# Kernel optimization log

Hardware: AMD Instinct MI355X
Metric: run time of the kernel (lower is better)

Reference implementation:

```python
import jax, jax.numpy as jnp
from jax import lax
import numpy as np

N = 227328   # B(32) * T(64) * 111 ROIs, block-diagonal collated graph
E = 1000000  # thresholded sparse edges
H = 128      # hidden_dim
NB = 111     # brain ROIs per graph (hardcoded in source)
P = 40       # |perm| (pooled node subset)
MAXLEN = 10  # max_path_length
NSTART = 5   # top-5 start nodes


def setup_inputs() -> dict:
    key = jax.random.key(0)
    ks = jax.random.split(key, 12)
    s = 1.0 / np.sqrt(H)
    return dict(
        v=jax.random.normal(ks[0], (N, H), jnp.float32),
        edge_row=jax.random.randint(ks[1], (E,), 0, N, jnp.int32),
        edge_col=jax.random.randint(ks[2], (E,), 0, N, jnp.int32),
        W1=jax.random.normal(ks[3], (H, H), jnp.float32) * s,
        b1=jnp.zeros((H,), jnp.float32),
        g1=jnp.ones((H,), jnp.float32),
        be1=jnp.zeros((H,), jnp.float32),
        W2=jax.random.normal(ks[4], (H, H), jnp.float32) * s,
        b2=jnp.zeros((H,), jnp.float32),
        g2=jnp.ones((H,), jnp.float32),
        be2=jnp.zeros((H,), jnp.float32),
        epsilon=jnp.zeros((1, 1), jnp.float32),
        adj111=jax.random.randint(ks[5], (NB, NB), 0, 2, jnp.int32),
        node_scores=jax.random.normal(ks[6], (NB,), jnp.float32),
        node_feats=jax.random.normal(ks[7], (NB, H), jnp.float32),
        perm=jnp.arange(P, dtype=jnp.int32),
        x_small=jax.random.normal(ks[8], (P, H), jnp.float32),
    )


def _batchnorm(x, g, b, eps=1e-5):
    # BatchNorm1d in training mode: biased batch statistics over node dim
    m = x.mean(0)
    var = x.var(0)
    return g * (x - m) * lax.rsqrt(var + eps) + b


def _gin(v, row, col, epsilon, W1, b1, g1, be1, W2, b2, g2, be2):
    # torch.sparse.mm(a, v): agg[i] = sum_{j: a[i,j]=1} v[j]
    agg = jax.ops.segment_sum(v[col], row, num_segments=v.shape[0])
    h = agg + epsilon[0, 0] * v
    h = jax.nn.relu(_batchnorm(h @ W1 + b1, g1, be1))
    h = jax.nn.relu(_batchnorm(h @ W2 + b2, g2, be2))
    return h


def _biased_random_walk(adj, scores, x, feats, perm):
    soft = jax.nn.softmax(scores)
    order = jnp.argsort(-scores)              # nodes by descending score
    in_perm = jnp.isin(order, perm)
    pos = jnp.where(in_perm, jnp.arange(NB), NB)
    starts = order[jnp.argsort(pos)[:NSTART]]  # first 5 sorted nodes in perm
    start_ok = jnp.arange(NSTART) < jnp.minimum(jnp.sum(in_perm), NSTART)

    def walk_one(carry, se):
        all_visited, xc = carry
        start, ok = se
        skip = jnp.logical_or(~ok, all_visited[start])
        visited0 = all_visited.at[start].set(True)

        def step(c, _):
            cur, visited, alive = c
            nbr = (adj[cur] > 0) & (~visited)
            has = jnp.any(nbr) & alive
            nxt = jnp.argmax(jnp.where(nbr, soft, -jnp.inf))  # greedy by softmax score
            cur2 = jnp.where(has, nxt, cur)
            visited2 = jnp.where(has, visited.at[nxt].set(True), visited)
            return (cur2, visited2, has), (cur2, has)

        (_, visited_f, _), (pn, pv) = lax.scan(
            step, (start, visited0, True), None, length=MAXLEN - 1)
        path = jnp.concatenate([start[None], pn])           # [MAXLEN]
        valid = jnp.concatenate([jnp.array([True]), pv])
        w = jax.nn.softmax(jnp.where(valid, scores[path], -jnp.inf))
        fused = jnp.sum(w[:, None] * feats[path], axis=0)   # [H]
        idx = jnp.argmax(perm == start)
        do = (~skip) & jnp.any(perm == start)
        x_new = jnp.where(do, xc.at[idx].add(fused), xc)
        av_new = jnp.where(skip, all_visited, visited_f)
        return (av_new, x_new), None

    (_, x_out), _ = lax.scan(
        walk_one, (jnp.zeros((NB,), bool), x), (starts, start_ok))
    return x_out


def reference(v, edge_row, edge_col, W1, b1, g1, be1, W2, b2, g2, be2,
              epsilon, adj111, node_scores, node_feats, perm, x_small):
    gin_out = _gin(v, edge_row, edge_col, epsilon,
                   W1, b1, g1, be1, W2, b2, g2, be2)
    x_fused = _biased_random_walk(adj111, node_scores, x_small,
                                  node_feats, perm)
    return gin_out, x_fused
```

## Files before the change

kernel.cpp:

```cpp
#include <hip/hip_runtime.h>
#include <hip/hip_bf16.h>
#include <math.h>

#define N_NODES 227328
#define H_DIM 128
#define NB_ 111
#define P_ 40
#define MAXLEN_ 10
#define NSTART_ 5
#define NH (N_NODES * H_DIM)
#define SCAN_BLK 1024

typedef __attribute__((ext_vector_type(8))) short short8;
typedef __attribute__((ext_vector_type(8))) unsigned short ushort8;
typedef __attribute__((ext_vector_type(4))) float f32x4;


__global__ __launch_bounds__(256) void k_zero(float* wsf, int* cnt, int n) {
    int gstride = gridDim.x * blockDim.x;
    for (int i = blockIdx.x * blockDim.x + threadIdx.x; i < n; i += gstride) cnt[i] = 0;
    if (blockIdx.x == 0)
        for (int i = threadIdx.x; i < 1280; i += 256) wsf[i] = 0.f;
}


__device__ inline unsigned short f2bf(float x) {
    unsigned u = __float_as_uint(x);
    return (unsigned short)((u + 0x7FFFu + ((u >> 16) & 1u)) >> 16);
}

__global__ __launch_bounds__(256) void k_conv(const float4* __restrict__ v4,
                                              ushort8* __restrict__ vb8, int n8) {
    int stride = gridDim.x * blockDim.x;
    for (int i = blockIdx.x * blockDim.x + threadIdx.x; i < n8; i += stride) {
        float4 a = v4[i * 2], b = v4[i * 2 + 1];
        ushort8 o;
        o[0] = f2bf(a.x); o[1] = f2bf(a.y); o[2] = f2bf(a.z); o[3] = f2bf(a.w);
        o[4] = f2bf(b.x); o[5] = f2bf(b.y); o[6] = f2bf(b.z); o[7] = f2bf(b.w);
        vb8[i] = o;
    }
}


__global__ __launch_bounds__(256) void k_hist(const int* __restrict__ erow, int* cnt, int E) {
    int stride = gridDim.x * blockDim.x;
    for (int e = blockIdx.x * blockDim.x + threadIdx.x; e < E; e += stride)
        atomicAdd(&cnt[erow[e]], 1);
}

__global__ __launch_bounds__(256) void k_scan1(const int* __restrict__ cnt, int* __restrict__ ptr,
                                               int* __restrict__ bsum, int n) {
    __shared__ int s_warp[4];
    int t = threadIdx.x;
    int base = blockIdx.x * SCAN_BLK + t * 4;
    int x0 = (base + 0 < n) ? cnt[base + 0] : 0;
    int x1 = (base + 1 < n) ? cnt[base + 1] : 0;
    int x2 = (base + 2 < n) ? cnt[base + 2] : 0;
    int x3 = (base + 3 < n) ? cnt[base + 3] : 0;
    int tsum = x0 + x1 + x2 + x3;
    int lane = t & 63, w = t >> 6;
    int v = tsum;
#pragma unroll
    for (int m = 1; m < 64; m <<= 1) {
        int o = __shfl_up(v, m, 64);
        if (lane >= m) v += o;
    }
    if (lane == 63) s_warp[w] = v;
    __syncthreads();
    int wadd = 0;
    for (int j = 0; j < w; j++) wadd += s_warp[j];
    int excl = v - tsum + wadd;
    if (base + 0 < n) ptr[base + 0] = excl;
    if (base + 1 < n) ptr[base + 1] = excl + x0;
    if (base + 2 < n) ptr[base + 2] = excl + x0 + x1;
    if (base + 3 < n) ptr[base + 3] = excl + x0 + x1 + x2;
    if (t == 0) bsum[blockIdx.x] = s_warp[0] + s_warp[1] + s_warp[2] + s_warp[3];
}

__global__ __launch_bounds__(256) void k_scan2(int* bsum, int nb) {
    __shared__ int s[256];
    int t = threadIdx.x;
    s[t] = (t < nb) ? bsum[t] : 0;
    __syncthreads();
    if (t == 0) {
        int acc = 0;
        for (int i = 0; i < nb; i++) { int x = s[i]; s[i] = acc; acc += x; }
    }
    __syncthreads();
    if (t < nb) bsum[t] = s[t];
}

__global__ __launch_bounds__(256) void k_scan3(int* __restrict__ ptr, const int* __restrict__ bsum,
                                               int* __restrict__ cur, int n, int E) {
    int stride = gridDim.x * blockDim.x;
    for (int i = blockIdx.x * blockDim.x + threadIdx.x; i < n; i += stride) {
        int p = ptr[i] + bsum[i / SCAN_BLK];
        ptr[i] = p;
        cur[i] = p;
    }
    if (blockIdx.x == 0 && threadIdx.x == 0) ptr[n] = E;
}

__global__ __launch_bounds__(256) void k_fill(const int* __restrict__ erow,
                                              const int* __restrict__ ecol,
                                              int* cur, int* __restrict__ col, int E) {
    int stride = gridDim.x * blockDim.x;
    for (int e = blockIdx.x * blockDim.x + threadIdx.x; e < E; e += stride) {
        int p = atomicAdd(&cur[erow[e]], 1);
        col[p] = ecol[e];
    }
}


__device__ inline float blo(unsigned u) { return __uint_as_float(u << 16); }
__device__ inline float bhi(unsigned u) { return __uint_as_float(u & 0xFFFF0000u); }

__global__ __launch_bounds__(256) void k_agg_bf16(const float* __restrict__ v,
                                                  const unsigned* __restrict__ vbu,
                                                  const int* __restrict__ ptr,
                                                  const int* __restrict__ col,
                                                  const float* __restrict__ epsp,
                                                  float* __restrict__ out, int n) {
    int r = (blockIdx.x * 256 + threadIdx.x) >> 6;
    int lane = threadIdx.x & 63;
    if (r >= n) return;
    float eps = epsp[0];
    float2 a = *((const float2*)(v + (size_t)r * H_DIM) + lane);
    float acx = eps * a.x, acy = eps * a.y;
    int s = ptr[r], e = ptr[r + 1];
    int i = s;
    for (; i + 8 <= e; i += 8) {
        unsigned u0 = vbu[(size_t)col[i + 0] * 64 + lane];
        unsigned u1 = vbu[(size_t)col[i + 1] * 64 + lane];
        unsigned u2 = vbu[(size_t)col[i + 2] * 64 + lane];
        unsigned u3 = vbu[(size_t)col[i + 3] * 64 + lane];
        unsigned u4 = vbu[(size_t)col[i + 4] * 64 + lane];
        unsigned u5 = vbu[(size_t)col[i + 5] * 64 + lane];
        unsigned u6 = vbu[(size_t)col[i + 6] * 64 + lane];
        unsigned u7 = vbu[(size_t)col[i + 7] * 64 + lane];
        acx += ((blo(u0) + blo(u1)) + (blo(u2) + blo(u3))) +
               ((blo(u4) + blo(u5)) + (blo(u6) + blo(u7)));
        acy += ((bhi(u0) + bhi(u1)) + (bhi(u2) + bhi(u3))) +
               ((bhi(u4) + bhi(u5)) + (bhi(u6) + bhi(u7)));
    }
    for (; i + 4 <= e; i += 4) {
        unsigned u0 = vbu[(size_t)col[i + 0] * 64 + lane];
        unsigned u1 = vbu[(size_t)col[i + 1] * 64 + lane];
        unsigned u2 = vbu[(size_t)col[i + 2] * 64 + lane];
        unsigned u3 = vbu[(size_t)col[i + 3] * 64 + lane];
        acx += (blo(u0) + blo(u1)) + (blo(u2) + blo(u3));
        acy += (bhi(u0) + bhi(u1)) + (bhi(u2) + bhi(u3));
    }
    for (; i < e; i++) {
        unsigned u = vbu[(size_t)col[i] * 64 + lane];
        acx += blo(u);
        acy += bhi(u);
    }
    *((float2*)(out + (size_t)r * H_DIM) + lane) = make_float2(acx, acy);
}

__global__ __launch_bounds__(256) void k_agg(const float* __restrict__ v,
                                             const int* __restrict__ ptr,
                                             const int* __restrict__ col,
                                             const float* __restrict__ epsp,
                                             float* __restrict__ out, int n) {
    int r = (blockIdx.x * 256 + threadIdx.x) >> 6;
    int lane = threadIdx.x & 63;
    if (r >= n) return;
    float eps = epsp[0];
    float2 a = *((const float2*)(v + (size_t)r * H_DIM) + lane);
    float acx = eps * a.x, acy = eps * a.y;
    int s = ptr[r], e = ptr[r + 1];
    int i = s;
    for (; i + 4 <= e; i += 4) {
        int c0 = col[i], c1 = col[i + 1], c2 = col[i + 2], c3 = col[i + 3];
        float2 b0 = *((const float2*)(v + (size_t)c0 * H_DIM) + lane);
        float2 b1 = *((const float2*)(v + (size_t)c1 * H_DIM) + lane);
        float2 b2 = *((const float2*)(v + (size_t)c2 * H_DIM) + lane);
        float2 b3 = *((const float2*)(v + (size_t)c3 * H_DIM) + lane);
        acx += (b0.x + b1.x) + (b2.x + b3.x);
        acy += (b0.y + b1.y) + (b2.y + b3.y);
    }
    for (; i < e; i++) {
        int c = col[i];
        float2 b = *((const float2*)(v + (size_t)c * H_DIM) + lane);
        acx += b.x;
        acy += b.y;
    }
    *((float2*)(out + (size_t)r * H_DIM) + lane) = make_float2(acx, acy);
}


__global__ __launch_bounds__(256) void k_init(const float4* __restrict__ v4,
                                              const float* __restrict__ epsp,
                                              float4* __restrict__ out4, int n4) {
    float eps = epsp[0];
    int stride = gridDim.x * blockDim.x;
    for (int i = blockIdx.x * blockDim.x + threadIdx.x; i < n4; i += stride) {
        float4 a = v4[i];
        out4[i] = make_float4(eps * a.x, eps * a.y, eps * a.z, eps * a.w);
    }
}

__global__ __launch_bounds__(256) void k_scatter(const float* __restrict__ v,
                                                 const int* __restrict__ erow,
                                                 const int* __restrict__ ecol,
                                                 float* agg, int E) {
    int tid = blockIdx.x * blockDim.x + threadIdx.x;
    int lane = tid & 63;
    int wave = tid >> 6;
    int nwaves = (gridDim.x * blockDim.x) >> 6;
    for (int e = wave; e < E; e += nwaves) {
        int r = erow[e], c = ecol[e];
        const float2 val = *((const float2*)(v + (size_t)c * H_DIM) + lane);
        float* dst = agg + (size_t)r * H_DIM + lane * 2;
        unsafeAtomicAdd(dst, val.x);
        unsafeAtomicAdd(dst + 1, val.y);
    }
}


template <int BN>
__global__ __launch_bounds__(256, 2) void k_gemm_mfma(
        const float* __restrict__ A, float* __restrict__ C,
        const float* __restrict__ W, const float* __restrict__ bias,
        const float* __restrict__ scl_in, const float* __restrict__ of_in,
        float* __restrict__ sums, float* __restrict__ sumsq) {
    __shared__ unsigned short Whi[128 * 136];
    __shared__ unsigned short Wlo[128 * 136];
    __shared__ float scof[256];
    __shared__ float stats[2][4][128];

    const int t = threadIdx.x;
    const int w = t >> 6;
    const int l = t & 63;
    const int n = l & 15;
    const int g = l >> 4;
    const size_t row0 = (size_t)blockIdx.x * 128 + w * 32;

    const float* Arow0 = A + (row0 + n) * H_DIM;
    const float* Arow1 = A + (row0 + 16 + n) * H_DIM;

    float4 x00 = *(const float4*)(Arow0 + g * 8);
    float4 x01 = *(const float4*)(Arow0 + g * 8 + 4);
    float4 x10 = *(const float4*)(Arow1 + g * 8);
    float4 x11 = *(const float4*)(Arow1 + g * 8 + 4);

#pragma unroll
    for (int it = 0; it < 8; ++it) {
        int p = it * 256 + t;
        int k = (p >> 5) * 2;
        int c = (p & 31) * 4;
        float4 wa = *(const float4*)(W + k * 128 + c);
        float4 wb = *(const float4*)(W + (k + 1) * 128 + c);
        float fa[4] = {wa.x, wa.y, wa.z, wa.w};
        float fb[4] = {wb.x, wb.y, wb.z, wb.w};
#pragma unroll
        for (int j = 0; j < 4; ++j) {
            unsigned ua = __float_as_uint(fa[j]);
            unsigned ub = __float_as_uint(fb[j]);
            unsigned ha = ua >> 16, hb = ub >> 16;
            float ra = fa[j] - __uint_as_float(ua & 0xFFFF0000u);
            float rb = fb[j] - __uint_as_float(ub & 0xFFFF0000u);
            unsigned la = __float_as_uint(ra) >> 16;
            unsigned lb = __float_as_uint(rb) >> 16;
            *(unsigned*)(&Whi[(c + j) * 136 + k]) = ha | (hb << 16);
            *(unsigned*)(&Wlo[(c + j) * 136 + k]) = la | (lb << 16);
        }
    }
    if (BN && t < 128) { scof[t] = scl_in[t]; scof[128 + t] = of_in[t]; }
    __syncthreads();

    float breg[8];
#pragma unroll
    for (int cb = 0; cb < 8; cb++) breg[cb] = bias[cb * 16 + n];

    f32x4 acc[2][8];
#pragma unroll
    for (int rf = 0; rf < 2; rf++)
#pragma unroll
        for (int cb = 0; cb < 8; cb++) acc[rf][cb] = (f32x4){0.f, 0.f, 0.f, 0.f};

#pragma unroll
    for (int kb = 0; kb < 4; kb++) {
        float4 y00, y01, y10, y11;
        if (kb < 3) {
            const int kn = (kb + 1) * 32 + g * 8;
            y00 = *(const float4*)(Arow0 + kn);
            y01 = *(const float4*)(Arow0 + kn + 4);
            y10 = *(const float4*)(Arow1 + kn);
            y11 = *(const float4*)(Arow1 + kn + 4);
        }
        const int k0 = kb * 32 + g * 8;
        float xs0[8] = {x00.x, x00.y, x00.z, x00.w, x01.x, x01.y, x01.z, x01.w};
        float xs1[8] = {x10.x, x10.y, x10.z, x10.w, x11.x, x11.y, x11.z, x11.w};
        if (BN) {
            float sc[8], of[8];
            float4 sa = *(const float4*)(scof + k0);
            float4 sb = *(const float4*)(scof + k0 + 4);
            float4 oa = *(const float4*)(scof + 128 + k0);
            float4 ob = *(const float4*)(scof + 128 + k0 + 4);
            sc[0] = sa.x; sc[1] = sa.y; sc[2] = sa.z; sc[3] = sa.w;
            sc[4] = sb.x; sc[5] = sb.y; sc[6] = sb.z; sc[7] = sb.w;
            of[0] = oa.x; of[1] = oa.y; of[2] = oa.z; of[3] = oa.w;
            of[4] = ob.x; of[5] = ob.y; of[6] = ob.z; of[7] = ob.w;
#pragma unroll
            for (int e = 0; e < 8; e++) {
                xs0[e] = fmaxf(fmaf(xs0[e], sc[e], of[e]), 0.f);
                xs1[e] = fmaxf(fmaf(xs1[e], sc[e], of[e]), 0.f);
            }
        }
        short8 ah0, al0, ah1, al1;
#pragma unroll
        for (int e = 0; e < 8; e++) {
            unsigned u0 = __float_as_uint(xs0[e]);
            ah0[e] = (short)(unsigned short)(u0 >> 16);
            al0[e] = (short)(unsigned short)(__float_as_uint(xs0[e] - __uint_as_float(u0 & 0xFFFF0000u)) >> 16);
            unsigned u1 = __float_as_uint(xs1[e]);
            ah1[e] = (short)(unsigned short)(u1 >> 16);
            al1[e] = (short)(unsigned short)(__float_as_uint(xs1[e] - __uint_as_float(u1 & 0xFFFF0000u)) >> 16);
        }

        short8 wh[8], wl[8];
        const int wb = n * 136 + kb * 32 + g * 8;
#pragma unroll
        for (int cb = 0; cb < 8; cb++) {
            wh[cb] = *(const short8*)(Whi + cb * 2176 + wb);
            wl[cb] = *(const short8*)(Wlo + cb * 2176 + wb);
        }
#pragma unroll
        for (int cb = 0; cb < 8; cb++) {
            acc[0][cb] = __builtin_amdgcn_mfma_f32_16x16x32_bf16(ah0, wh[cb], acc[0][cb], 0, 0, 0);
            acc[1][cb] = __builtin_amdgcn_mfma_f32_16x16x32_bf16(ah1, wh[cb], acc[1][cb], 0, 0, 0);
            acc[0][cb] = __builtin_amdgcn_mfma_f32_16x16x32_bf16(al0, wh[cb], acc[0][cb], 0, 0, 0);
            acc[1][cb] = __builtin_amdgcn_mfma_f32_16x16x32_bf16(al1, wh[cb], acc[1][cb], 0, 0, 0);
            acc[0][cb] = __builtin_amdgcn_mfma_f32_16x16x32_bf16(ah0, wl[cb], acc[0][cb], 0, 0, 0);
            acc[1][cb] = __builtin_amdgcn_mfma_f32_16x16x32_bf16(ah1, wl[cb], acc[1][cb], 0, 0, 0);
        }
        x00 = y00; x01 = y01; x10 = y10; x11 = y11;
    }

    float s[8], s2[8];
#pragma unroll
    for (int cb = 0; cb < 8; cb++) { s[cb] = 0.f; s2[cb] = 0.f; }
#pragma unroll
    for (int cb = 0; cb < 8; cb++) {
        const int c = cb * 16 + n;
#pragma unroll
        for (int rf = 0; rf < 2; rf++) {
            f32x4 o = acc[rf][cb];
            const size_t rbase = (row0 + rf * 16 + g * 4) * H_DIM + c;
#pragma unroll
            for (int r = 0; r < 4; r++) {
                float val = o[r] + breg[cb];
                C[rbase + (size_t)r * H_DIM] = val;
                s[cb] += val;
                s2[cb] += val * val;
            }
        }
    }
#pragma unroll
    for (int cb = 0; cb < 8; cb++) {
        s[cb] += __shfl_xor(s[cb], 16, 64);
        s[cb] += __shfl_xor(s[cb], 32, 64);
        s2[cb] += __shfl_xor(s2[cb], 16, 64);
        s2[cb] += __shfl_xor(s2[cb], 32, 64);
    }
    if (g == 0) {
#pragma unroll
        for (int cb = 0; cb < 8; cb++) {
            stats[0][w][cb * 16 + n] = s[cb];
            stats[1][w][cb * 16 + n] = s2[cb];
        }
    }
    __syncthreads();
    if (t < 128) {
        float S  = stats[0][0][t] + stats[0][1][t] + stats[0][2][t] + stats[0][3][t];
        float S2 = stats[1][0][t] + stats[1][1][t] + stats[1][2][t] + stats[1][3][t];
        unsafeAtomicAdd(sums + t, S);
        unsafeAtomicAdd(sumsq + t, S2);
    }
}

__global__ void k_finalize(const float* __restrict__ sums, const float* __restrict__ sumsq,
                           float* __restrict__ mean, float* __restrict__ scl,
                           float* __restrict__ of,
                           const float* __restrict__ g, const float* __restrict__ beta,
                           float invN) {
    int t = threadIdx.x;
    if (t < H_DIM) {
        float m = sums[t] * invN;
        float var = sumsq[t] * invN - m * m;
        float sc = g[t] * rsqrtf(var + 1e-5f);
        mean[t] = m;
        scl[t] = sc;
        of[t] = beta[t] - m * sc;
    }
}


__device__ inline float block_max4(float v, int t, float* s_r) {
#pragma unroll
    for (int m = 1; m < 64; m <<= 1) v = fmaxf(v, __shfl_xor(v, m, 64));
    if ((t & 63) == 0) s_r[t >> 6] = v;
    __syncthreads();
    float r = fmaxf(fmaxf(s_r[0], s_r[1]), fmaxf(s_r[2], s_r[3]));
    __syncthreads();
    return r;
}

__device__ inline float block_sum4(float v, int t, float* s_r) {
#pragma unroll
    for (int m = 1; m < 64; m <<= 1) v += __shfl_xor(v, m, 64);
    if ((t & 63) == 0) s_r[t >> 6] = v;
    __syncthreads();
    float r = (s_r[0] + s_r[1]) + (s_r[2] + s_r[3]);
    __syncthreads();
    return r;
}

__device__ inline void block_argmax4(float v, int idx, int t, float* s_rv, int* s_ri,
                                     float* outv, int* outi) {
#pragma unroll
    for (int m = 1; m < 64; m <<= 1) {
        float ov = __shfl_xor(v, m, 64);
        int oi = __shfl_xor(idx, m, 64);
        if (ov > v || (ov == v && oi < idx)) { v = ov; idx = oi; }
    }
    if ((t & 63) == 0) { s_rv[t >> 6] = v; s_ri[t >> 6] = idx; }
    __syncthreads();
    float bv = s_rv[0];
    int bi = s_ri[0];
#pragma unroll
    for (int j = 1; j < 4; j++) {
        float ov = s_rv[j];
        int oi = s_ri[j];
        if (ov > bv || (ov == bv && oi < bi)) { bv = ov; bi = oi; }
    }
    *outv = bv;
    *outi = bi;
    __syncthreads();
}

__global__ __launch_bounds__(256) void k_bnwalk(
        float4* y4, const float* __restrict__ scl, const float* __restrict__ of, int n4,
        const int* __restrict__ adj, const float* __restrict__ scores,
        const float* __restrict__ feats, const int* __restrict__ perm,
        const float* __restrict__ xs, float* __restrict__ outw) {
    __shared__ int s_adj[NB_ * NB_];
    __shared__ float s_scores[NB_], s_soft[NB_];
    __shared__ int s_perm[P_];
    __shared__ unsigned char s_inperm[NB_], s_sel[NB_], s_allvis[NB_], s_vis[NB_];
    __shared__ int s_starts[NSTART_];
    __shared__ int s_path[MAXLEN_];
    __shared__ unsigned char s_valid[MAXLEN_];
    __shared__ float s_w[MAXLEN_];
    __shared__ int s_cur, s_alive, s_do, s_idx, s_skip;
    __shared__ float s_rv[4];
    __shared__ int s_ri[4];

    const int t = threadIdx.x;

    if (blockIdx.x != 0) {
        int stride = (gridDim.x - 1) * 256;
        for (int i = (blockIdx.x - 1) * 256 + t; i < n4; i += stride) {
            int c = (i & 31) * 4;
            float4 a = y4[i];
            a.x = fmaxf(fmaf(a.x, scl[c + 0], of[c + 0]), 0.f);
            a.y = fmaxf(fmaf(a.y, scl[c + 1], of[c + 1]), 0.f);
            a.z = fmaxf(fmaf(a.z, scl[c + 2], of[c + 2]), 0.f);
            a.w = fmaxf(fmaf(a.w, scl[c + 3], of[c + 3]), 0.f);
            y4[i] = a;
        }
        return;
    }

    for (int i = t; i < P_ * H_DIM; i += 256) outw[i] = xs[i];
    for (int i = t; i < NB_ * NB_; i += 256) s_adj[i] = adj[i];
    if (t < P_) s_perm[t] = perm[t];
    if (t < NB_) { s_scores[t] = scores[t]; s_allvis[t] = 0; s_sel[t] = 0; }
    __syncthreads();
    if (t < NB_) {
        unsigned char inp = 0;
        for (int j = 0; j < P_; j++) inp |= (s_perm[j] == t) ? 1 : 0;
        s_inperm[t] = inp;
    }
    __syncthreads();

    float myv = (t < NB_) ? s_scores[t] : -INFINITY;
    float mx = block_max4(myv, t, s_rv);
    float e = (t < NB_) ? expf(s_scores[t] - mx) : 0.f;
    float ssum = block_sum4(e, t, s_rv);
    if (t < NB_) s_soft[t] = e / ssum;

    float ninf = block_sum4((t < NB_ && s_inperm[t]) ? 1.f : 0.f, t, s_rv);
    int nin = (int)(ninf + 0.5f);
    int nok = nin < NSTART_ ? nin : NSTART_;
    __syncthreads();

    for (int r = 0; r < NSTART_; r++) {
        bool useIn = (r < nin);
        bool elig = (t < NB_) && !s_sel[t] && (((s_inperm[t] != 0)) == useIn);
        float v = elig ? s_scores[t] : -INFINITY;
        float mv; int mi;
        block_argmax4(v, elig ? t : 0x7fffffff, t, s_rv, s_ri, &mv, &mi);
        if (t == 0) s_starts[r] = mi;
        if (t == mi && t < NB_) s_sel[t] = 1;
        __syncthreads();
    }

    for (int s = 0; s < NSTART_; s++) {
        if (t == 0) {
            int start = s_starts[s];
            int ok = (s < nok) ? 1 : 0;
            int skip = (!ok) || s_allvis[start];
            s_skip = skip;
            s_cur = start;
            s_alive = 1;
            s_path[0] = start;
            s_valid[0] = 1;
            int idx = 0, found = 0;
            for (int j = 0; j < P_; j++)
                if (!found && s_perm[j] == start) { idx = j; found = 1; }
            s_idx = idx;
            s_do = (!skip) && found;
        }
        __syncthreads();
        if (t < NB_) s_vis[t] = s_allvis[t];
        __syncthreads();
        if (t == 0) s_vis[s_cur] = 1;
        __syncthreads();

        for (int st = 1; st < MAXLEN_; st++) {
            int cur = s_cur;
            int alive = s_alive;
            bool elig = (t < NB_) && alive && (s_adj[cur * NB_ + t] > 0) && (!s_vis[t]);
            float v = elig ? s_soft[t] : -INFINITY;
            float mv; int mi;
            block_argmax4(v, elig ? t : 0x7fffffff, t, s_rv, s_ri, &mv, &mi);
            if (t == 0) {
                int has = (mv > -INFINITY) ? 1 : 0;
                if (has) { s_cur = mi; s_vis[mi] = 1; }
                s_path[st] = has ? mi : cur;
                s_valid[st] = (unsigned char)has;
                s_alive = has;
            }
            __syncthreads();
        }

        if (t == 0) {
            float mxw = -INFINITY;
            for (int st = 0; st < MAXLEN_; st++)
                if (s_valid[st]) mxw = fmaxf(mxw, s_scores[s_path[st]]);
            float sw = 0.f;
            for (int st = 0; st < MAXLEN_; st++) {
                float ev = s_valid[st] ? expf(s_scores[s_path[st]] - mxw) : 0.f;
                s_w[st] = ev; sw += ev;
            }
            float inv = 1.f / sw;
            for (int st = 0; st < MAXLEN_; st++) s_w[st] *= inv;
        }
        __syncthreads();
        if (s_do && t < H_DIM) {
            float acc = 0.f;
            for (int st = 0; st < MAXLEN_; st++)
                acc += s_w[st] * feats[s_path[st] * H_DIM + t];
            outw[s_idx * H_DIM + t] += acc;
        }
        __syncthreads();
        if (!s_skip && t < NB_) s_allvis[t] = s_vis[t];
        __syncthreads();
    }
}


extern "C" void kernel_launch(void* const* d_in, const int* in_sizes, int n_in,
                              void* d_out, int out_size, void* d_ws, size_t ws_size,
                              hipStream_t stream) {
    const float* v    = (const float*)d_in[0];
    const int*   erow = (const int*)d_in[1];
    const int*   ecol = (const int*)d_in[2];
    const float* W1   = (const float*)d_in[3];
    const float* b1   = (const float*)d_in[4];
    const float* g1   = (const float*)d_in[5];
    const float* be1  = (const float*)d_in[6];
    const float* W2   = (const float*)d_in[7];
    const float* b2   = (const float*)d_in[8];
    const float* g2   = (const float*)d_in[9];
    const float* be2  = (const float*)d_in[10];
    const float* epsp = (const float*)d_in[11];
    const int*   adj  = (const int*)d_in[12];
    const float* scr  = (const float*)d_in[13];
    const float* fts  = (const float*)d_in[14];
    const int*   perm = (const int*)d_in[15];
    const float* xs   = (const float*)d_in[16];

    float* out = (float*)d_out;
    float* wsf = (float*)d_ws;
    float* sums1 = wsf,        *sumsq1 = wsf + 128,  *mean1 = wsf + 256,  *scl1 = wsf + 384,  *of1 = wsf + 512;
    float* sums2 = wsf + 640,  *sumsq2 = wsf + 768,  *mean2 = wsf + 896,  *scl2 = wsf + 1024, *of2 = wsf + 1152;

    const int E  = in_sizes[1];
    const int N  = N_NODES;
    const int n4 = NH / 4;

    int* ws_i = (int*)(wsf + 1280);
    int* cnt  = ws_i;
    int* ptr  = ws_i + (N + 1);
    int* cur  = ws_i + 2 * (N + 1);
    int* col  = ws_i + 3 * (N + 1);
    size_t need_csr = 1280 * 4 + (size_t)(3 * (N + 1) + E) * 4;
    size_t off_vb   = (need_csr + 15) & ~(size_t)15;
    size_t need_vb  = off_vb + (size_t)NH * 2;
    unsigned* vbu = (unsigned*)((char*)d_ws + off_vb);

    if (ws_size >= need_csr) {
        const int nb = (N + SCAN_BLK - 1) / SCAN_BLK;
        k_zero<<<512, 256, 0, stream>>>(wsf, cnt, N + 1);
        bool useBf = (ws_size >= need_vb);
        if (useBf)
            k_conv<<<2048, 256, 0, stream>>>((const float4*)v, (ushort8*)vbu, NH / 8);
        k_hist<<<1024, 256, 0, stream>>>(erow, cnt, E);
        k_scan1<<<nb, 256, 0, stream>>>(cnt, ptr, cur , N);
        k_scan2<<<1, 256, 0, stream>>>(cur, nb);
        k_scan3<<<512, 256, 0, stream>>>(ptr, cur, cnt , N, E);
        k_fill<<<1024, 256, 0, stream>>>(erow, ecol, cnt, col, E);
        if (useBf)
            k_agg_bf16<<<N / 4, 256, 0, stream>>>(v, vbu, ptr, col, epsp, out, N);
        else
            k_agg<<<N / 4, 256, 0, stream>>>(v, ptr, col, epsp, out, N);
    } else {
        k_zero<<<512, 256, 0, stream>>>(wsf, cnt, 0);
        k_init<<<2048, 256, 0, stream>>>((const float4*)v, epsp, (float4*)out, n4);
        k_scatter<<<4096, 256, 0, stream>>>(v, erow, ecol, out, E);
    }

    k_gemm_mfma<0><<<N / 128, 256, 0, stream>>>(out, out, W1, b1, nullptr, nullptr,
                                                sums1, sumsq1);
    k_finalize<<<1, 128, 0, stream>>>(sums1, sumsq1, mean1, scl1, of1, g1, be1, 1.f / N);
    k_gemm_mfma<1><<<N / 128, 256, 0, stream>>>(out, out, W2, b2, scl1, of1,
                                                sums2, sumsq2);
    k_finalize<<<1, 128, 0, stream>>>(sums2, sumsq2, mean2, scl2, of2, g2, be2, 1.f / N);
    k_bnwalk<<<2049, 256, 0, stream>>>((float4*)out, scl2, of2, n4,
                                       adj, scr, fts, perm, xs, out + NH);
}
```

Before: 712.9 us.

## Fuse histogram into bf16 conversion, simplify GEMM loads, bitmask adjacency in walk

Merges the edge-count histogram into the bf16 conversion kernel, removing one launch. The GEMM now stages W with scalar per-element loads instead of vectorized float4 loads, and reads A inside the k-loop instead of prefetching the next slice. The random walk packs the 111x111 adjacency into per-row 64-bit bitmasks, shrinking shared memory. The GEMM changes may lose load latency hiding and load efficiency, while the fusion and bitmask changes trim launch overhead and shared-memory use.

Measured after the change: 675.0 us. 5.3% less time.

```diff
diff --git a/kernel.cpp b/kernel.cpp
--- a/kernel.cpp
+++ b/kernel.cpp
@@ -29,24 +29,22 @@
     return (unsigned short)((u + 0x7FFFu + ((u >> 16) & 1u)) >> 16);
 }
 
-__global__ __launch_bounds__(256) void k_conv(const float4* __restrict__ v4,
-                                              ushort8* __restrict__ vb8, int n8) {
+__global__ __launch_bounds__(256) void k_hist_conv(const int* __restrict__ erow, int* cnt, int E,
+                                                   const float4* __restrict__ v4,
+                                                   ushort8* __restrict__ vb8, int n8) {
     int stride = gridDim.x * blockDim.x;
-    for (int i = blockIdx.x * blockDim.x + threadIdx.x; i < n8; i += stride) {
+    int tid = blockIdx.x * blockDim.x + threadIdx.x;
+    for (int i = tid; i < n8; i += stride) {
         float4 a = v4[i * 2], b = v4[i * 2 + 1];
         ushort8 o;
         o[0] = f2bf(a.x); o[1] = f2bf(a.y); o[2] = f2bf(a.z); o[3] = f2bf(a.w);
         o[4] = f2bf(b.x); o[5] = f2bf(b.y); o[6] = f2bf(b.z); o[7] = f2bf(b.w);
         vb8[i] = o;
     }
-}
-
-
-__global__ __launch_bounds__(256) void k_hist(const int* __restrict__ erow, int* cnt, int E) {
-    int stride = gridDim.x * blockDim.x;
-    for (int e = blockIdx.x * blockDim.x + threadIdx.x; e < E; e += stride)
+    for (int e = tid; e < E; e += stride)
         atomicAdd(&cnt[erow[e]], 1);
 }
+
 
 __global__ __launch_bounds__(256) void k_scan1(const int* __restrict__ cnt, int* __restrict__ ptr,
                                                int* __restrict__ bsum, int n) {
@@ -220,6 +218,16 @@
 }
 
 
+__device__ inline void split8(const float* xs, short8& hi, short8& lo) {
+#pragma unroll
+    for (int e = 0; e < 8; e++) {
+        unsigned u = __float_as_uint(xs[e]);
+        hi[e] = (short)(unsigned short)(u >> 16);
+        float hf = __uint_as_float(u & 0xFFFF0000u);
+        lo[e] = (short)(unsigned short)(__float_as_uint(xs[e] - hf) >> 16);
+    }
+}
+
 template <int BN>
 __global__ __launch_bounds__(256, 2) void k_gemm_mfma(
         const float* __restrict__ A, float* __restrict__ C,
@@ -238,60 +246,39 @@
     const int g = l >> 4;
     const size_t row0 = (size_t)blockIdx.x * 128 + w * 32;
 
+#pragma unroll 8
+    for (int it = 0; it < 64; ++it) {
+        int k = it * 2 + (t >> 7);
+        int nn = t & 127;
+        float wv = W[k * 128 + nn];
+        unsigned u = __float_as_uint(wv);
+        Whi[nn * 136 + k] = (unsigned short)(u >> 16);
+        float hf = __uint_as_float(u & 0xFFFF0000u);
+        Wlo[nn * 136 + k] = (unsigned short)(__float_as_uint(wv - hf) >> 16);
+    }
+    if (BN && t < 128) { scof[t] = scl_in[t]; scof[128 + t] = of_in[t]; }
+    __syncthreads();
+
+    float breg[8];
+#pragma unroll
+    for (int cb = 0; cb < 8; cb++) breg[cb] = bias[cb * 16 + n];
+
+    f32x4 acc[2][8];
+#pragma unroll
+    for (int rf = 0; rf < 2; rf++)
+#pragma unroll
+        for (int cb = 0; cb < 8; cb++) acc[rf][cb] = (f32x4){0.f, 0.f, 0.f, 0.f};
+
     const float* Arow0 = A + (row0 + n) * H_DIM;
     const float* Arow1 = A + (row0 + 16 + n) * H_DIM;
 
-    float4 x00 = *(const float4*)(Arow0 + g * 8);
-    float4 x01 = *(const float4*)(Arow0 + g * 8 + 4);
-    float4 x10 = *(const float4*)(Arow1 + g * 8);
-    float4 x11 = *(const float4*)(Arow1 + g * 8 + 4);
-
-#pragma unroll
-    for (int it = 0; it < 8; ++it) {
-        int p = it * 256 + t;
-        int k = (p >> 5) * 2;
-        int c = (p & 31) * 4;
-        float4 wa = *(const float4*)(W + k * 128 + c);
-        float4 wb = *(const float4*)(W + (k + 1) * 128 + c);
-        float fa[4] = {wa.x, wa.y, wa.z, wa.w};
-        float fb[4] = {wb.x, wb.y, wb.z, wb.w};
-#pragma unroll
-        for (int j = 0; j < 4; ++j) {
-            unsigned ua = __float_as_uint(fa[j]);
-            unsigned ub = __float_as_uint(fb[j]);
-            unsigned ha = ua >> 16, hb = ub >> 16;
-            float ra = fa[j] - __uint_as_float(ua & 0xFFFF0000u);
-            float rb = fb[j] - __uint_as_float(ub & 0xFFFF0000u);
-            unsigned la = __float_as_uint(ra) >> 16;
-            unsigned lb = __float_as_uint(rb) >> 16;
-            *(unsigned*)(&Whi[(c + j) * 136 + k]) = ha | (hb << 16);
-            *(unsigned*)(&Wlo[(c + j) * 136 + k]) = la | (lb << 16);
-        }
-    }
-    if (BN && t < 128) { scof[t] = scl_in[t]; scof[128 + t] = of_in[t]; }
-    __syncthreads();
-
-    float breg[8];
-#pragma unroll
-    for (int cb = 0; cb < 8; cb++) breg[cb] = bias[cb * 16 + n];
-
-    f32x4 acc[2][8];
-#pragma unroll
-    for (int rf = 0; rf < 2; rf++)
-#pragma unroll
-        for (int cb = 0; cb < 8; cb++) acc[rf][cb] = (f32x4){0.f, 0.f, 0.f, 0.f};
-
 #pragma unroll
     for (int kb = 0; kb < 4; kb++) {
-        float4 y00, y01, y10, y11;
-        if (kb < 3) {
-            const int kn = (kb + 1) * 32 + g * 8;
-            y00 = *(const float4*)(Arow0 + kn);
-            y01 = *(const float4*)(Arow0 + kn + 4);
-            y10 = *(const float4*)(Arow1 + kn);
-            y11 = *(const float4*)(Arow1 + kn + 4);
-        }
         const int k0 = kb * 32 + g * 8;
+        float4 x00 = *(const float4*)(Arow0 + k0);
+        float4 x01 = *(const float4*)(Arow0 + k0 + 4);
+        float4 x10 = *(const float4*)(Arow1 + k0);
+        float4 x11 = *(const float4*)(Arow1 + k0 + 4);
         float xs0[8] = {x00.x, x00.y, x00.z, x00.w, x01.x, x01.y, x01.z, x01.w};
         float xs1[8] = {x10.x, x10.y, x10.z, x10.w, x11.x, x11.y, x11.z, x11.w};
         if (BN) {
@@ -311,15 +298,8 @@
             }
         }
         short8 ah0, al0, ah1, al1;
-#pragma unroll
-        for (int e = 0; e < 8; e++) {
-            unsigned u0 = __float_as_uint(xs0[e]);
-            ah0[e] = (short)(unsigned short)(u0 >> 16);
-            al0[e] = (short)(unsigned short)(__float_as_uint(xs0[e] - __uint_as_float(u0 & 0xFFFF0000u)) >> 16);
-            unsigned u1 = __float_as_uint(xs1[e]);
-            ah1[e] = (short)(unsigned short)(u1 >> 16);
-            al1[e] = (short)(unsigned short)(__float_as_uint(xs1[e] - __uint_as_float(u1 & 0xFFFF0000u)) >> 16);
-        }
+        split8(xs0, ah0, al0);
+        split8(xs1, ah1, al1);
 
         short8 wh[8], wl[8];
         const int wb = n * 136 + kb * 32 + g * 8;
@@ -337,7 +317,6 @@
             acc[0][cb] = __builtin_amdgcn_mfma_f32_16x16x32_bf16(ah0, wl[cb], acc[0][cb], 0, 0, 0);
             acc[1][cb] = __builtin_amdgcn_mfma_f32_16x16x32_bf16(ah1, wl[cb], acc[1][cb], 0, 0, 0);
         }
-        x00 = y00; x01 = y01; x10 = y10; x11 = y11;
     }
 
     float s[8], s2[8];
@@ -447,7 +426,7 @@
         const int* __restrict__ adj, const float* __restrict__ scores,
         const float* __restrict__ feats, const int* __restrict__ perm,
         const float* __restrict__ xs, float* __restrict__ outw) {
-    __shared__ int s_adj[NB_ * NB_];
+    __shared__ unsigned long long s_am0[NB_], s_am1[NB_];
     __shared__ float s_scores[NB_], s_soft[NB_];
     __shared__ int s_perm[P_];
     __shared__ unsigned char s_inperm[NB_], s_sel[NB_], s_allvis[NB_], s_vis[NB_];
@@ -476,9 +455,17 @@
     }
 
     for (int i = t; i < P_ * H_DIM; i += 256) outw[i] = xs[i];
-    for (int i = t; i < NB_ * NB_; i += 256) s_adj[i] = adj[i];
     if (t < P_) s_perm[t] = perm[t];
     if (t < NB_) { s_scores[t] = scores[t]; s_allvis[t] = 0; s_sel[t] = 0; }
+    if (t < NB_) {
+        const int* row = adj + t * NB_;
+        unsigned long long m0 = 0ull, m1 = 0ull;
+#pragma unroll
+        for (int j = 0; j < 64; j++) m0 |= (unsigned long long)(row[j] > 0 ? 1u : 0u) << j;
+        for (int j = 64; j < NB_; j++) m1 |= (unsigned long long)(row[j] > 0 ? 1u : 0u) << (j - 64);
+        s_am0[t] = m0;
+        s_am1[t] = m1;
+    }
     __syncthreads();
     if (t < NB_) {
         unsigned char inp = 0;
@@ -534,7 +521,9 @@
         for (int st = 1; st < MAXLEN_; st++) {
             int cur = s_cur;
             int alive = s_alive;
-            bool elig = (t < NB_) && alive && (s_adj[cur * NB_ + t] > 0) && (!s_vis[t]);
+            int abit = (t < 64) ? (int)((s_am0[cur] >> t) & 1ull)
+                                : (int)((s_am1[cur] >> (t - 64)) & 1ull);
+            bool elig = (t < NB_) && alive && abit && (!s_vis[t]);
             float v = elig ? s_soft[t] : -INFINITY;
             float mv; int mi;
             block_argmax4(v, elig ? t : 0x7fffffff, t, s_rv, s_ri, &mv, &mi);
@@ -616,11 +605,14 @@
 
     if (ws_size >= need_csr) {
         const int nb = (N + SCAN_BLK - 1) / SCAN_BLK;
+        bool useBf = (ws_size >= need_vb);
         k_zero<<<512, 256, 0, stream>>>(wsf, cnt, N + 1);
-        bool useBf = (ws_size >= need_vb);
         if (useBf)
-            k_conv<<<2048, 256, 0, stream>>>((const float4*)v, (ushort8*)vbu, NH / 8);
-        k_hist<<<1024, 256, 0, stream>>>(erow, cnt, E);
+            k_hist_conv<<<2048, 256, 0, stream>>>(erow, cnt, E, (const float4*)v,
+                                                  (ushort8*)vbu, NH / 8);
+        else
+            k_hist_conv<<<2048, 256, 0, stream>>>(erow, cnt, E, (const float4*)v,
+                                                  (ushort8*)vbu, 0);
         k_scan1<<<nb, 256, 0, stream>>>(cnt, ptr, cur , N);
         k_scan2<<<1, 256, 0, stream>>>(cur, nb);
         k_scan3<<<512, 256, 0, stream>>>(ptr, cur, cnt , N, E);
```
